# Kernel optimization log

Hardware: AMD Instinct MI355X
Metric: run time of the kernel (lower is better)

Reference implementation:

```python
import jax, jax.numpy as jnp
import numpy as np


def setup_inputs() -> dict:
    key = jax.random.key(0)
    x = jax.random.normal(key, (4, 256, 64, 64), dtype=jnp.float32)
    return {"x": x}


def reference(x):
    b, c, h, w = x.shape
    n = h * w
    v = x.reshape(b, c, n)                     # [b, c, N]
    # energy[b, i, j] = sum_c x[b, c, i] * x[b, c, j]  (Q = K = V = flattened x)
    energy = jnp.einsum('bci,bcj->bij', v, v)  # [b, N, N]
    attn = jax.nn.softmax(energy, axis=-1)
    # out[b, c, i] = sum_j v[b, c, j] * attn[b, i, j]  (bmm(V, attn^T))
    out = jnp.einsum('bcj,bij->bci', v, attn)
    return out.reshape(b, c, h, w)
```

## Files before the change

### kernel.cpp

```cpp
#include <hip/hip_runtime.h>
#include <hip/hip_bf16.h>

typedef __bf16 bf16x8 __attribute__((ext_vector_type(8)));
typedef float f32x4 __attribute__((ext_vector_type(4)));

#define NB 4
#define NC 256
#define NN 4096
#define BK 32
#define NT 64

__device__ __forceinline__ void stage16(const void* g, void* l) {
    __builtin_amdgcn_global_load_lds(
        (const __attribute__((address_space(1))) unsigned int*)g,
        (__attribute__((address_space(3))) unsigned int*)l, 16, 0, 0);
}

__global__ __launch_bounds__(256) void prep_kernel(const float* __restrict__ x,
                                                   __bf16* __restrict__ xt,
                                                   __bf16* __restrict__ xc) {
    __shared__ __align__(16) __bf16 tile[64 * 64];
    const int b = blockIdx.z, c0 = blockIdx.y * 64, n0 = blockIdx.x * 64;
    const int t = threadIdx.x;
    {
        const int cc = t >> 2, nch = (t & 3) << 4;
        const float* src = x + ((size_t)(b * NC + c0 + cc)) * NN + n0 + nch;
        f32x4 v[4];
        v[0] = *(const f32x4*)(src);
        v[1] = *(const f32x4*)(src + 4);
        v[2] = *(const f32x4*)(src + 8);
        v[3] = *(const f32x4*)(src + 12);
        bf16x8 o[2];
#pragma unroll
        for (int q = 0; q < 2; ++q)
#pragma unroll
            for (int k = 0; k < 8; ++k)
                o[q][k] = (__bf16)v[q * 2 + (k >> 2)][k & 3];
        __bf16* dst = xc + ((size_t)(b * NC + c0 + cc)) * NN + n0 + nch;
        *(bf16x8*)(dst) = o[0];
        *(bf16x8*)(dst + 8) = o[1];
        const int key = (cc ^ (cc >> 3)) & 7;
#pragma unroll
        for (int q = 0; q < 2; ++q) {
            int nc = (nch >> 3) + q;
            *(bf16x8*)(&tile[cc * 64 + ((nc ^ key) << 3)]) = o[q];
        }
    }
    __syncthreads();
    {
        const int nn = t >> 2, cch = (t & 3) << 4;
        bf16x8 o[2];
#pragma unroll
        for (int k = 0; k < 16; ++k) {
            int r = cch + k;
            int key = (r ^ (r >> 3)) & 7;
            o[k >> 3][k & 7] = tile[r * 64 + (((nn >> 3) ^ key) << 3) + (nn & 7)];
        }
        __bf16* dst = xt + ((size_t)(b * NN + n0 + nn)) * NC + c0 + cch;
        *(bf16x8*)(dst) = o[0];
        *(bf16x8*)(dst + 8) = o[1];
    }
}

__global__ __launch_bounds__(512, 2) void flash_kernel(const __bf16* __restrict__ xt,
                                                       const __bf16* __restrict__ xc,
                                                       float* __restrict__ out) {
    __shared__ __align__(16) __bf16 sK[2][2][BK * NC];
    __shared__ __align__(16) __bf16 sV[2][2][NC * BK];
    __shared__ __align__(16) __bf16 sP[8][16 * BK];
    __shared__ float sML[8][16][2];

    const int bid = blockIdx.x;
    const int b = (bid & 7) >> 1;
    const int qblk = ((bid >> 3) << 1) | (bid & 1);

    const int tid = threadIdx.x;
    const int w = tid >> 6;
    const int grp = w >> 2;
    const int wg = w & 3;
    const int lane = tid & 63;
    const int l16 = lane & 15;
    const int gq = lane >> 4;

    const int i_base = qblk * 64 + wg * 16;

    const char* xtb = (const char*)(xt + (size_t)b * NN * NC);
    const char* xcb = (const char*)(xc + (size_t)b * NC * NN);

    bf16x8 qf[8];
    {
        const __bf16* qrow = (const __bf16*)xtb + (size_t)(i_base + l16) * NC + gq * 8;
#pragma unroll
        for (int ck = 0; ck < 8; ++ck) qf[ck] = *(const bf16x8*)(qrow + ck * 32);
    }

    f32x4 acc[16];
#pragma unroll
    for (int cf = 0; cf < 16; ++cf) acc[cf] = (f32x4){0.f, 0.f, 0.f, 0.f};
    float m_run[4], l_run[4];
#pragma unroll
    for (int r = 0; r < 4; ++r) { m_run[r] = -3.0e38f; l_run[r] = 0.f; }

    auto stage = [&](int bf, int t) {
        const int tj = grp * NT + t;
        const char* kb = xtb + (size_t)tj * BK * (NC * 2);
        __bf16* dk = &sK[grp][bf][0];
#pragma unroll
        for (int q = 0; q < 4; ++q) {
            int ci = wg * 4 + q;
            int rl = ci * 2 + (lane >> 5);
            int cs = (lane & 31) ^ (rl & 7);
            stage16(kb + rl * 512 + cs * 16, dk + ci * 512);
        }
        const char* vb = xcb + (size_t)tj * (BK * 2);
        __bf16* dv = &sV[grp][bf][0];
#pragma unroll
        for (int q = 0; q < 4; ++q) {
            int ci = wg * 4 + q;
            int c = ci * 16 + (lane >> 2);
            int cs = (lane & 3) ^ ((c >> 1) & 3);
            stage16(vb + (size_t)c * (NN * 2) + cs * 16, dv + ci * 512);
        }
    };

    stage(0, 0);
    __syncthreads();
    int cur = 0;

    for (int t = 0; t < NT; ++t) {
        if (t + 1 < NT) stage(cur ^ 1, t + 1);

        const __bf16* kt = &sK[grp][cur][0];
        const __bf16* vt = &sV[grp][cur][0];

        f32x4 s0 = (f32x4){0.f, 0.f, 0.f, 0.f};
        f32x4 s1 = (f32x4){0.f, 0.f, 0.f, 0.f};
#pragma unroll
        for (int ck = 0; ck < 8; ++ck) {
            int q = ck * 4 + gq;
            bf16x8 k0 = *(const bf16x8*)(kt + l16 * 256 + ((q ^ (l16 & 7)) << 3));
            s0 = __builtin_amdgcn_mfma_f32_16x16x32_bf16(qf[ck], k0, s0, 0, 0, 0);
            int row1 = 16 + l16;
            bf16x8 k1 = *(const bf16x8*)(kt + row1 * 256 + ((q ^ (row1 & 7)) << 3));
            s1 = __builtin_amdgcn_mfma_f32_16x16x32_bf16(qf[ck], k1, s1, 0, 0, 0);
        }

        float vmax[4];
#pragma unroll
        for (int r = 0; r < 4; ++r) {
            float v = fmaxf(s0[r], s1[r]);
            v = fmaxf(v, __shfl_xor(v, 1));
            v = fmaxf(v, __shfl_xor(v, 2));
            v = fmaxf(v, __shfl_xor(v, 4));
            v = fmaxf(v, __shfl_xor(v, 8));
            vmax[r] = v;
        }
        bool grow = (vmax[0] > m_run[0]) || (vmax[1] > m_run[1]) ||
                    (vmax[2] > m_run[2]) || (vmax[3] > m_run[3]);
        if (__any((int)grow)) {
#pragma unroll
            for (int r = 0; r < 4; ++r) {
                float nm = fmaxf(m_run[r], vmax[r]);
                float sc = __expf(m_run[r] - nm);
                m_run[r] = nm;
                l_run[r] *= sc;
#pragma unroll
                for (int cf = 0; cf < 16; ++cf) acc[cf][r] *= sc;
            }
        }
        float p0[4], p1[4];
#pragma unroll
        for (int r = 0; r < 4; ++r) {
            p0[r] = __expf(s0[r] - m_run[r]);
            p1[r] = __expf(s1[r] - m_run[r]);
            float v = p0[r] + p1[r];
            v += __shfl_xor(v, 1);
            v += __shfl_xor(v, 2);
            v += __shfl_xor(v, 4);
            v += __shfl_xor(v, 8);
            l_run[r] += v;
        }

        __bf16* myP = &sP[w][0];
#pragma unroll
        for (int r = 0; r < 4; ++r) {
            int i = gq * 4 + r;
            int key = (i >> 1) & 3;
            myP[i * 32 + (((l16 >> 3) ^ key) << 3) + (l16 & 7)] = (__bf16)p0[r];
            int j1 = 16 + l16;
            myP[i * 32 + (((j1 >> 3) ^ key) << 3) + (j1 & 7)] = (__bf16)p1[r];
        }
        bf16x8 pa = *(const bf16x8*)(&myP[l16 * 32 + ((gq ^ ((l16 >> 1) & 3)) << 3)]);

#pragma unroll
        for (int cf = 0; cf < 16; ++cf) {
            int c = cf * 16 + l16;
            bf16x8 bv = *(const bf16x8*)(vt + c * 32 + ((gq ^ ((c >> 1) & 3)) << 3));
            acc[cf] = __builtin_amdgcn_mfma_f32_16x16x32_bf16(pa, bv, acc[cf], 0, 0, 0);
        }

        __syncthreads();
        cur ^= 1;
    }

    if (l16 == 0) {
#pragma unroll
        for (int r = 0; r < 4; ++r) {
            sML[w][gq * 4 + r][0] = m_run[r];
            sML[w][gq * 4 + r][1] = l_run[r];
        }
    }
    if (w >= 4) {
        float* F = ((float*)&sK[0][0][0]) + (size_t)(w - 4) * 4096;
#pragma unroll
        for (int cf = 0; cf < 16; ++cf)
#pragma unroll
            for (int r = 0; r < 4; ++r)
                F[cf * 256 + (gq * 4 + r) * 16 + l16] = acc[cf][r];
    }
    __syncthreads();
    if (w < 4) {
        const float* F = ((float*)&sK[0][0][0]) + (size_t)w * 4096;
        float sA[4], sB[4], inv[4];
#pragma unroll
        for (int r = 0; r < 4; ++r) {
            int i = gq * 4 + r;
            float mA = m_run[r], lA = l_run[r];
            float mB = sML[w + 4][i][0], lB = sML[w + 4][i][1];
            float m = fmaxf(mA, mB);
            float eA = __expf(mA - m), eB = __expf(mB - m);
            sA[r] = eA; sB[r] = eB;
            inv[r] = 1.f / (lA * eA + lB * eB);
        }
        float* sT = (float*)((char*)&sV[0][0][0] + (size_t)w * 4096);
#pragma unroll
        for (int cf = 0; cf < 16; ++cf) {
#pragma unroll
            for (int r = 0; r < 4; ++r) {
                float o = (acc[cf][r] * sA[r] +
                           F[cf * 256 + (gq * 4 + r) * 16 + l16] * sB[r]) * inv[r];
                sT[(gq * 4 + r) * 17 + l16] = o;
            }
#pragma unroll
            for (int r = 0; r < 4; ++r) {
                int c = cf * 16 + gq + r * 4;
                out[((size_t)(b * NC + c)) * NN + i_base + l16] = sT[l16 * 17 + gq + r * 4];
            }
        }
    }
}

extern "C" void kernel_launch(void* const* d_in, const int* in_sizes, int n_in,
                              void* d_out, int out_size, void* d_ws, size_t ws_size,
                              hipStream_t stream) {
    const float* x = (const float*)d_in[0];
    float* out = (float*)d_out;
    __bf16* xt = (__bf16*)d_ws;
    __bf16* xc = xt + (size_t)NB * NN * NC;

    prep_kernel<<<dim3(NN / 64, NC / 64, NB), dim3(256), 0, stream>>>(x, xt, xc);
    flash_kernel<<<dim3(256), dim3(512), 0, stream>>>(xt, xc, out);
}
```

Measured before the change: 242.2 us.

## Load V tiles directly from global into registers and halve block size

V tiles no longer go through double-buffered LDS staging. Each wave now reads its V fragments straight from global memory into registers every iteration. The block shrinks from 8 to 4 waves covering 32 query rows, and the grid doubles to 512 blocks. This frees LDS so two blocks can fit per CU, but K and V are now re-read for every 32 query rows instead of every 64, and the V global loads are issued inside the loop without any prefetch.

```diff
diff --git a/kernel.cpp b/kernel.cpp
--- a/kernel.cpp
+++ b/kernel.cpp
@@ -62,30 +62,30 @@
     }
 }
 
-__global__ __launch_bounds__(512, 2) void flash_kernel(const __bf16* __restrict__ xt,
+__global__ __launch_bounds__(256, 2) void flash_kernel(const __bf16* __restrict__ xt,
                                                        const __bf16* __restrict__ xc,
                                                        float* __restrict__ out) {
     __shared__ __align__(16) __bf16 sK[2][2][BK * NC];
-    __shared__ __align__(16) __bf16 sV[2][2][NC * BK];
-    __shared__ __align__(16) __bf16 sP[8][16 * BK];
-    __shared__ float sML[8][16][2];
+    __shared__ __align__(16) __bf16 sP[4][16 * BK];
+    __shared__ float sML[4][16][2];
 
     const int bid = blockIdx.x;
-    const int b = (bid & 7) >> 1;
-    const int qblk = ((bid >> 3) << 1) | (bid & 1);
+    const int xcd = bid & 7;
+    const int b = xcd >> 1;
+    const int qblk = ((bid >> 3) << 1) | (xcd & 1);
 
     const int tid = threadIdx.x;
     const int w = tid >> 6;
-    const int grp = w >> 2;
-    const int wg = w & 3;
+    const int grp = w >> 1;
+    const int wg = w & 1;
     const int lane = tid & 63;
     const int l16 = lane & 15;
     const int gq = lane >> 4;
 
-    const int i_base = qblk * 64 + wg * 16;
+    const int i_base = qblk * 32 + wg * 16;
 
     const char* xtb = (const char*)(xt + (size_t)b * NN * NC);
-    const char* xcb = (const char*)(xc + (size_t)b * NC * NN);
+    const __bf16* vbase = xc + (size_t)b * NC * NN;
 
     bf16x8 qf[8];
     {
@@ -106,32 +106,31 @@
         const char* kb = xtb + (size_t)tj * BK * (NC * 2);
         __bf16* dk = &sK[grp][bf][0];
 #pragma unroll
-        for (int q = 0; q < 4; ++q) {
-            int ci = wg * 4 + q;
+        for (int q = 0; q < 8; ++q) {
+            int ci = wg * 8 + q;
             int rl = ci * 2 + (lane >> 5);
             int cs = (lane & 31) ^ (rl & 7);
             stage16(kb + rl * 512 + cs * 16, dk + ci * 512);
         }
-        const char* vb = xcb + (size_t)tj * (BK * 2);
-        __bf16* dv = &sV[grp][bf][0];
-#pragma unroll
-        for (int q = 0; q < 4; ++q) {
-            int ci = wg * 4 + q;
-            int c = ci * 16 + (lane >> 2);
-            int cs = (lane & 3) ^ ((c >> 1) & 3);
-            stage16(vb + (size_t)c * (NN * 2) + cs * 16, dv + ci * 512);
-        }
     };
 
     stage(0, 0);
     __syncthreads();
     int cur = 0;
 
+    const __bf16* vrow = vbase + (size_t)l16 * NN + gq * 8;
+
     for (int t = 0; t < NT; ++t) {
         if (t + 1 < NT) stage(cur ^ 1, t + 1);
 
+        const int j0 = (grp * NT + t) * BK;
+
+        bf16x8 vv[16];
+#pragma unroll
+        for (int cf = 0; cf < 16; ++cf)
+            vv[cf] = *(const bf16x8*)(vrow + (size_t)cf * 16 * NN + j0);
+
         const __bf16* kt = &sK[grp][cur][0];
-        const __bf16* vt = &sV[grp][cur][0];
 
         f32x4 s0 = (f32x4){0.f, 0.f, 0.f, 0.f};
         f32x4 s1 = (f32x4){0.f, 0.f, 0.f, 0.f};
@@ -193,11 +192,8 @@
         bf16x8 pa = *(const bf16x8*)(&myP[l16 * 32 + ((gq ^ ((l16 >> 1) & 3)) << 3)]);
 
 #pragma unroll
-        for (int cf = 0; cf < 16; ++cf) {
-            int c = cf * 16 + l16;
-            bf16x8 bv = *(const bf16x8*)(vt + c * 32 + ((gq ^ ((c >> 1) & 3)) << 3));
-            acc[cf] = __builtin_amdgcn_mfma_f32_16x16x32_bf16(pa, bv, acc[cf], 0, 0, 0);
-        }
+        for (int cf = 0; cf < 16; ++cf)
+            acc[cf] = __builtin_amdgcn_mfma_f32_16x16x32_bf16(pa, vv[cf], acc[cf], 0, 0, 0);
 
         __syncthreads();
         cur ^= 1;
@@ -210,8 +206,8 @@
             sML[w][gq * 4 + r][1] = l_run[r];
         }
     }
-    if (w >= 4) {
-        float* F = ((float*)&sK[0][0][0]) + (size_t)(w - 4) * 4096;
+    if (w >= 2) {
+        float* F = ((float*)&sK[0][0][0]) + (size_t)(w - 2) * 4096;
 #pragma unroll
         for (int cf = 0; cf < 16; ++cf)
 #pragma unroll
@@ -219,20 +215,20 @@
                 F[cf * 256 + (gq * 4 + r) * 16 + l16] = acc[cf][r];
     }
     __syncthreads();
-    if (w < 4) {
+    if (w < 2) {
         const float* F = ((float*)&sK[0][0][0]) + (size_t)w * 4096;
         float sA[4], sB[4], inv[4];
 #pragma unroll
         for (int r = 0; r < 4; ++r) {
             int i = gq * 4 + r;
             float mA = m_run[r], lA = l_run[r];
-            float mB = sML[w + 4][i][0], lB = sML[w + 4][i][1];
+            float mB = sML[w + 2][i][0], lB = sML[w + 2][i][1];
             float m = fmaxf(mA, mB);
             float eA = __expf(mA - m), eB = __expf(mB - m);
             sA[r] = eA; sB[r] = eB;
             inv[r] = 1.f / (lA * eA + lB * eB);
         }
-        float* sT = (float*)((char*)&sV[0][0][0] + (size_t)w * 4096);
+        float* sT = ((float*)&sP[0][0]) + (size_t)w * 288;
 #pragma unroll
         for (int cf = 0; cf < 16; ++cf) {
 #pragma unroll
@@ -259,5 +255,5 @@
     __bf16* xc = xt + (size_t)NB * NN * NC;
 
     prep_kernel<<<dim3(NN / 64, NC / 64, NB), dim3(256), 0, stream>>>(x, xt, xc);
-    flash_kernel<<<dim3(256), dim3(512), 0, stream>>>(xt, xc, out);
-}
+    flash_kernel<<<dim3(512), dim3(256), 0, stream>>>(xt, xc, out);
+}
```

Measured after the change: 335.3 us. +38.5%, slower.
